# Performance work log

Hardware: AMD Instinct MI355X
Metric: run time of the kernel (lower is better)

Reference implementation:

```python
import jax, jax.numpy as jnp
import numpy as np

B, QL, KL = 8, 2048, 2048
QD, KD, ED = 1024, 1024, 1024


def setup_inputs() -> dict:
    key = jax.random.key(0)
    ks = jax.random.split(key, 11)
    s = 0.02
    return {
        "query": jax.random.normal(ks[0], (B, QL, QD), jnp.float32),
        "key_value": jax.random.normal(ks[1], (B, KL, KD), jnp.float32),
        "mask": jnp.ones((B, QL, KL), jnp.int32),
        "Wq": jax.random.normal(ks[2], (QD, ED), jnp.float32) * s,
        "bq": jnp.zeros((ED,), jnp.float32),
        "Wk": jax.random.normal(ks[3], (KD, ED), jnp.float32) * s,
        "bk": jnp.zeros((ED,), jnp.float32),
        "Wv": jax.random.normal(ks[4], (KD, ED), jnp.float32) * s,
        "bv": jnp.zeros((ED,), jnp.float32),
        "Wo": jax.random.normal(ks[5], (ED, ED), jnp.float32) * s,
        "bo": jnp.zeros((ED,), jnp.float32),
    }


def reference(query, key_value, mask, Wq, bq, Wk, bk, Wv, bv, Wo, bo):
    # Linear projections
    Q = jnp.einsum('bqd,de->bqe', query, Wq) + bq      # (B, QL, E)
    K = jnp.einsum('bkd,de->bke', key_value, Wk) + bk  # (B, KL, E)
    V = jnp.einsum('bkd,de->bke', key_value, Wv) + bv  # (B, KL, E)
    scale = 1.0 / jnp.sqrt(jnp.asarray(Q.shape[-1], Q.dtype))
    scores = jnp.einsum('bqe,bke->bqk', Q, K) * scale  # (B, QL, KL)
    scores = jnp.where(mask == 0, -jnp.inf, scores)
    attn = jax.nn.softmax(scores, axis=-1)             # (B, QL, KL)
    # dropout is identity in eval mode
    attended = jnp.einsum('bqk,bke->bqe', attn, V)     # (B, QL, E)
    out = jnp.einsum('bqe,ef->bqf', attended, Wo) + bo
    return out, attn
```

## Files before the change

### kernel.cpp

```cpp
#include <hip/hip_runtime.h>
#include <hip/hip_bf16.h>
#include <math.h>


typedef __attribute__((ext_vector_type(8))) short short8;
typedef __attribute__((ext_vector_type(4))) float floatx4;

__device__ __forceinline__ unsigned short f2bf(float x) {
  return __builtin_bit_cast(unsigned short, __float2bfloat16(x));
}
__device__ __forceinline__ float bf2f(unsigned short s) {
  unsigned int u = ((unsigned int)s) << 16;
  return __builtin_bit_cast(float, u);
}

typedef const unsigned int __attribute__((address_space(1))) ga_u32;
typedef unsigned int __attribute__((address_space(3))) lds_u32;
__device__ __forceinline__ void gl_lds16(const void* g, void* l) {
  __builtin_amdgcn_global_load_lds((ga_u32*)g, (lds_u32*)l, 16, 0, 0);
}

template <int EPI>
__global__ __launch_bounds__(512, 2) void gemm8(
    const unsigned short* __restrict__ Ah,
    const unsigned short* __restrict__ Bh, void* __restrict__ Cp,
    const float* __restrict__ bias, float alpha, int M, int N, int K, int Mt,
    long long sA, long long sB, long long sC) {
  extern __shared__ char smem[];

  const int gx = gridDim.x;
  const int gxy = gx * gridDim.y;
  const int nwg = gxy * gridDim.z;
  const int orig = blockIdx.z * gxy + blockIdx.y * gx + blockIdx.x;
  const int wg = (orig & 7) * (nwg >> 3) + (orig >> 3);
  const int zb_i = wg / gxy;
  const int rem = wg - zb_i * gxy;
  const int by = rem / gx;
  const int bx = rem - by * gx;
  const int m0 = by * 256, n0 = bx * 256;
  const long long zb = zb_i;

  const unsigned short* Ag = Ah + zb * sA;
  const unsigned short* Bg = Bh + zb * sB;

  const int t = threadIdx.x;
  const int srow = t >> 3;
  const int skw = ((t & 7) << 3) ^ ((srow & 7) << 3);
  const unsigned short* aS = Ag + (long long)(m0 + srow) * K + skw;
  const unsigned short* bS = Bg + (long long)(n0 + srow) * K + skw;
  char* dstA = smem + t * 16;
  char* dstB = smem + 65536 + t * 16;

  const int lane = t & 63;
  const int wv = t >> 6, wy = wv >> 2, wx = wv & 3;
  const int lm = lane & 15, q = lane >> 4;
  const int x0 = (q << 4) ^ ((lm & 7) << 4);
  const int aB0 = (wy * 128 + lm) * 128;
  const int bB0 = 65536 + (wx * 64 + lm) * 128;
  const int aRd0 = aB0 + x0, aRd1 = aB0 + (x0 ^ 64);
  const int bRd0 = bB0 + x0, bRd1 = bB0 + (x0 ^ 64);

  floatx4 acc[8][4];
#pragma unroll
  for (int i = 0; i < 8; ++i)
#pragma unroll
    for (int j = 0; j < 4; ++j) acc[i][j] = (floatx4)(0.0f);

  short8 fa[4][2];
  short8 fb[2][2][2];

#pragma unroll
  for (int c = 0; c < 4; ++c) {
    gl_lds16(aS + (long long)(c * 64) * K, dstA + c * 8192);
    gl_lds16(bS + (long long)(c * 64) * K, dstB + c * 8192);
  }
  gl_lds16(aS + 64, dstA + 32768);
  gl_lds16(bS + 64, dstB + 32768);
  gl_lds16(aS + 64LL * K + 64, dstA + 32768 + 8192);
  gl_lds16(bS + 64LL * K + 64, dstB + 32768 + 8192);
  asm volatile("s_waitcnt vmcnt(4)" ::: "memory");
  __builtin_amdgcn_s_barrier();

  auto tile = [&](int kt, int bo, int nbo) {
    const bool p1 = (kt + 64) < K;
    const bool p2 = (kt + 128) < K;
#pragma unroll
    for (int mt = 0; mt < 4; ++mt) {
      fa[mt][0] = *(const short8*)(smem + (bo + aRd0 + mt * 2048));
      fa[mt][1] = *(const short8*)(smem + (bo + aRd1 + mt * 2048));
    }
#pragma unroll
    for (int nt = 0; nt < 2; ++nt) {
      fb[0][nt][0] = *(const short8*)(smem + (bo + bRd0 + nt * 2048));
      fb[0][nt][1] = *(const short8*)(smem + (bo + bRd1 + nt * 2048));
    }
    if (p1) {
      gl_lds16(aS + 128LL * K + (kt + 64), dstA + nbo + 16384);
      gl_lds16(bS + 128LL * K + (kt + 64), dstB + nbo + 16384);
    }
    __builtin_amdgcn_s_barrier();
    __builtin_amdgcn_s_setprio(1);
#pragma unroll
    for (int mt = 0; mt < 4; ++mt)
#pragma unroll
      for (int nt = 0; nt < 2; ++nt) {
        acc[mt][nt] = __builtin_amdgcn_mfma_f32_16x16x32_bf16(
            fa[mt][0], fb[0][nt][0], acc[mt][nt], 0, 0, 0);
        acc[mt][nt] = __builtin_amdgcn_mfma_f32_16x16x32_bf16(
            fa[mt][1], fb[0][nt][1], acc[mt][nt], 0, 0, 0);
      }
    __builtin_amdgcn_s_setprio(0);
    __builtin_amdgcn_s_barrier();
#pragma unroll
    for (int nt = 0; nt < 2; ++nt) {
      fb[1][nt][0] = *(const short8*)(smem + (bo + bRd0 + 4096 + nt * 2048));
      fb[1][nt][1] = *(const short8*)(smem + (bo + bRd1 + 4096 + nt * 2048));
    }
    if (p1) {
      gl_lds16(aS + 192LL * K + (kt + 64), dstA + nbo + 24576);
      gl_lds16(bS + 192LL * K + (kt + 64), dstB + nbo + 24576);
    }
    __builtin_amdgcn_s_barrier();
    __builtin_amdgcn_s_setprio(1);
#pragma unroll
    for (int mt = 0; mt < 4; ++mt)
#pragma unroll
      for (int nt = 0; nt < 2; ++nt) {
        acc[mt][2 + nt] = __builtin_amdgcn_mfma_f32_16x16x32_bf16(
            fa[mt][0], fb[1][nt][0], acc[mt][2 + nt], 0, 0, 0);
        acc[mt][2 + nt] = __builtin_amdgcn_mfma_f32_16x16x32_bf16(
            fa[mt][1], fb[1][nt][1], acc[mt][2 + nt], 0, 0, 0);
      }
    __builtin_amdgcn_s_setprio(0);
    __builtin_amdgcn_s_barrier();
#pragma unroll
    for (int mt = 0; mt < 4; ++mt) {
      fa[mt][0] = *(const short8*)(smem + (bo + aRd0 + 8192 + mt * 2048));
      fa[mt][1] = *(const short8*)(smem + (bo + aRd1 + 8192 + mt * 2048));
    }
    if (p2) {
      gl_lds16(aS + (kt + 128), dstA + bo);
      gl_lds16(bS + (kt + 128), dstB + bo);
    }
    __builtin_amdgcn_s_barrier();
    __builtin_amdgcn_s_setprio(1);
#pragma unroll
    for (int mt = 0; mt < 4; ++mt)
#pragma unroll
      for (int nt = 0; nt < 2; ++nt) {
        acc[4 + mt][nt] = __builtin_amdgcn_mfma_f32_16x16x32_bf16(
            fa[mt][0], fb[0][nt][0], acc[4 + mt][nt], 0, 0, 0);
        acc[4 + mt][nt] = __builtin_amdgcn_mfma_f32_16x16x32_bf16(
            fa[mt][1], fb[0][nt][1], acc[4 + mt][nt], 0, 0, 0);
      }
    __builtin_amdgcn_s_setprio(0);
    __builtin_amdgcn_s_barrier();
    if (p2) {
      gl_lds16(aS + 64LL * K + (kt + 128), dstA + bo + 8192);
      gl_lds16(bS + 64LL * K + (kt + 128), dstB + bo + 8192);
    }
    __builtin_amdgcn_s_barrier();
    __builtin_amdgcn_s_setprio(1);
#pragma unroll
    for (int mt = 0; mt < 4; ++mt)
#pragma unroll
      for (int nt = 0; nt < 2; ++nt) {
        acc[4 + mt][2 + nt] = __builtin_amdgcn_mfma_f32_16x16x32_bf16(
            fa[mt][0], fb[1][nt][0], acc[4 + mt][2 + nt], 0, 0, 0);
        acc[4 + mt][2 + nt] = __builtin_amdgcn_mfma_f32_16x16x32_bf16(
            fa[mt][1], fb[1][nt][1], acc[4 + mt][2 + nt], 0, 0, 0);
      }
    __builtin_amdgcn_s_setprio(0);
    if (p2) {
      asm volatile("s_waitcnt vmcnt(4)" ::: "memory");
    } else {
      asm volatile("s_waitcnt vmcnt(0)" ::: "memory");
    }
    __builtin_amdgcn_s_barrier();
  };

  for (int kt = 0; kt < K; kt += 128) {
    tile(kt, 0, 32768);
    tile(kt + 64, 32768, 0);
  }

#pragma unroll
  for (int ni = 0; ni < 4; ++ni) {
    const int col = n0 + wx * 64 + ni * 16 + lm;
    const float bvv = bias ? bias[col] : 0.0f;
#pragma unroll
    for (int mi = 0; mi < 8; ++mi) {
      const int rbase = m0 + wy * 128 + mi * 16 + q * 4;
      if constexpr (EPI == 3) {
        const int b = rbase / Mt;
        const int kk = rbase - b * Mt;
        unsigned short* dd =
            (unsigned short*)Cp + (long long)b * sC + (long long)col * Mt + kk;
        ushort4 pk;
        pk.x = f2bf(acc[mi][ni][0] * alpha + bvv);
        pk.y = f2bf(acc[mi][ni][1] * alpha + bvv);
        pk.z = f2bf(acc[mi][ni][2] * alpha + bvv);
        pk.w = f2bf(acc[mi][ni][3] * alpha + bvv);
        *reinterpret_cast<ushort4*>(dd) = pk;
      } else {
#pragma unroll
        for (int i = 0; i < 4; ++i) {
          const long long idx = zb * sC + (long long)(rbase + i) * N + col;
          const float x = acc[mi][ni][i] * alpha + bvv;
          if constexpr (EPI == 0) {
            ((float*)Cp)[idx] = x;
          } else {
            ((unsigned short*)Cp)[idx] = f2bf(x);
          }
        }
      }
    }
  }
}

__global__ __launch_bounds__(256) void cvt_bf16(const float* __restrict__ in,
                                                unsigned short* __restrict__ o,
                                                int n8) {
  const int i = blockIdx.x * 256 + threadIdx.x;
  if (i >= n8) return;
  const float4* p = reinterpret_cast<const float4*>(in) + (long long)i * 2;
  const float4 a = p[0], b = p[1];
  short8 h;
  h[0] = (short)f2bf(a.x); h[1] = (short)f2bf(a.y);
  h[2] = (short)f2bf(a.z); h[3] = (short)f2bf(a.w);
  h[4] = (short)f2bf(b.x); h[5] = (short)f2bf(b.y);
  h[6] = (short)f2bf(b.z); h[7] = (short)f2bf(b.w);
  reinterpret_cast<short8*>(o)[i] = h;
}

__global__ __launch_bounds__(256) void prep_w(const float* __restrict__ W,
                                              unsigned short* __restrict__ Th,
                                              int R, int C) {
  __shared__ float tile[32][33];
  const int c0 = blockIdx.x * 32, r0 = blockIdx.y * 32;
  const int tx = threadIdx.x & 31, ty = threadIdx.x >> 5;
#pragma unroll
  for (int i = 0; i < 4; ++i)
    tile[ty + i * 8][tx] = W[(long long)(r0 + ty + i * 8) * C + c0 + tx];
  __syncthreads();
#pragma unroll
  for (int i = 0; i < 4; ++i) {
    const float x = tile[tx][ty + i * 8];
    const long long idx = (long long)(c0 + ty + i * 8) * R + r0 + tx;
    Th[idx] = f2bf(x);
  }
}

__global__ __launch_bounds__(256) void bias_wo(const float* __restrict__ bv,
                                               const float* __restrict__ Wo,
                                               float* __restrict__ bvWo) {
  __shared__ float red[4][64];
  const int fl = threadIdx.x & 63, eg = threadIdx.x >> 6;
  const int f = blockIdx.x * 64 + fl;
  float s = 0.0f;
  const int e0 = eg * 256;
  for (int e = e0; e < e0 + 256; ++e)
    s += bv[e] * Wo[(long long)e * 1024 + f];
  red[eg][fl] = s;
  __syncthreads();
  if (eg == 0) bvWo[f] = red[0][fl] + red[1][fl] + red[2][fl] + red[3][fl];
}

__device__ __forceinline__ float wave_max64(float v) {
#pragma unroll
  for (int o = 32; o > 0; o >>= 1) v = fmaxf(v, __shfl_xor(v, o, 64));
  return v;
}
__device__ __forceinline__ float wave_sum64(float v) {
#pragma unroll
  for (int o = 32; o > 0; o >>= 1) v += __shfl_xor(v, o, 64);
  return v;
}

__global__ __launch_bounds__(256) void softmax_kernel(
    const unsigned short* __restrict__ Sh, const int* __restrict__ mask,
    float* __restrict__ attn, unsigned short* __restrict__ Ph) {
  const long long base = (long long)blockIdx.x * 2048;
  const int t = threadIdx.x;

  float vals[8];
  float lmax = -INFINITY;
#pragma unroll
  for (int g = 0; g < 2; ++g) {
    const int idx = (t + g * 256) * 4;
    const uint2 u = *reinterpret_cast<const uint2*>(Sh + base + idx);
    const int4 m = *reinterpret_cast<const int4*>(mask + base + idx);
    vals[g * 4 + 0] = m.x ? bf2f((unsigned short)(u.x & 0xffff)) : -INFINITY;
    vals[g * 4 + 1] = m.y ? bf2f((unsigned short)(u.x >> 16)) : -INFINITY;
    vals[g * 4 + 2] = m.z ? bf2f((unsigned short)(u.y & 0xffff)) : -INFINITY;
    vals[g * 4 + 3] = m.w ? bf2f((unsigned short)(u.y >> 16)) : -INFINITY;
  }
#pragma unroll
  for (int i = 0; i < 8; ++i) lmax = fmaxf(lmax, vals[i]);

  __shared__ float red[4];
  const float wm = wave_max64(lmax);
  if ((t & 63) == 0) red[t >> 6] = wm;
  __syncthreads();
  const float rmax = fmaxf(fmaxf(red[0], red[1]), fmaxf(red[2], red[3]));
  __syncthreads();

  float lsum = 0.0f;
#pragma unroll
  for (int i = 0; i < 8; ++i) {
    const float e = __expf(vals[i] - rmax);
    vals[i] = e;
    lsum += e;
  }
  const float wsum = wave_sum64(lsum);
  if ((t & 63) == 0) red[t >> 6] = wsum;
  __syncthreads();
  const float inv = 1.0f / (red[0] + red[1] + red[2] + red[3]);

#pragma unroll
  for (int g = 0; g < 2; ++g) {
    const int idx = (t + g * 256) * 4;
    float4 o;
    o.x = vals[g * 4 + 0] * inv;
    o.y = vals[g * 4 + 1] * inv;
    o.z = vals[g * 4 + 2] * inv;
    o.w = vals[g * 4 + 3] * inv;
    *reinterpret_cast<float4*>(attn + base + idx) = o;
    uint2 p;
    p.x = (unsigned)f2bf(o.x) | ((unsigned)f2bf(o.y) << 16);
    p.y = (unsigned)f2bf(o.z) | ((unsigned)f2bf(o.w) << 16);
    *reinterpret_cast<uint2*>(Ph + base + idx) = p;
  }
}

extern "C" void kernel_launch(void* const* d_in, const int* in_sizes, int n_in,
                              void* d_out, int out_size, void* d_ws,
                              size_t ws_size, hipStream_t stream) {
  const float* query = (const float*)d_in[0];
  const float* keyv = (const float*)d_in[1];
  const int* mask = (const int*)d_in[2];
  const float* Wq = (const float*)d_in[3];
  const float* bq = (const float*)d_in[4];
  const float* Wk = (const float*)d_in[5];
  const float* bk = (const float*)d_in[6];
  const float* Wv = (const float*)d_in[7];
  const float* bv = (const float*)d_in[8];
  const float* Wo = (const float*)d_in[9];
  const float* bo = (const float*)d_in[10];

  const int B = 8, QL = 2048, KL = 2048, D = 1024;
  const long long ML = (long long)B * QL;

  static int inited = 0;
  if (!inited) {
    hipFuncSetAttribute(reinterpret_cast<const void*>(&gemm8<0>),
                        hipFuncAttributeMaxDynamicSharedMemorySize, 131072);
    hipFuncSetAttribute(reinterpret_cast<const void*>(&gemm8<1>),
                        hipFuncAttributeMaxDynamicSharedMemorySize, 131072);
    hipFuncSetAttribute(reinterpret_cast<const void*>(&gemm8<3>),
                        hipFuncAttributeMaxDynamicSharedMemorySize, 131072);
    inited = 1;
  }

  float* out = (float*)d_out;
  float* attn = out + ML * D;

  char* w = (char*)d_ws;
  unsigned short* Qh = (unsigned short*)(w);
  unsigned short* Kh = (unsigned short*)(w + (32ll << 20));
  unsigned short* KVf = (unsigned short*)(w + (64ll << 20));
  unsigned short* Qf = (unsigned short*)(w + (96ll << 20));
  unsigned short* VWoT = (unsigned short*)(w + (128ll << 20));
  unsigned short* Sh = (unsigned short*)(w + (64ll << 20));
  unsigned short* Ph = (unsigned short*)(w);
  unsigned short* WqT = (unsigned short*)(w + (160ll << 20));
  unsigned short* WkT = WqT + (1ll << 20);
  unsigned short* WoTh = WkT + (1ll << 20);
  unsigned short* W2T = WoTh + (1ll << 20);
  unsigned short* WvH = W2T + (1ll << 20);
  float* bvWo = attn;

  const dim3 blk(256);
  const int n8 = (int)(ML * D / 8);

  cvt_bf16<<<dim3(n8 / 256), blk, 0, stream>>>(query, Qf, n8);
  cvt_bf16<<<dim3(n8 / 256), blk, 0, stream>>>(keyv, KVf, n8);
  cvt_bf16<<<dim3(512), blk, 0, stream>>>(Wv, WvH, D * D / 8);

  prep_w<<<dim3(32, 32), blk, 0, stream>>>(Wq, WqT, D, D);
  prep_w<<<dim3(32, 32), blk, 0, stream>>>(Wk, WkT, D, D);
  prep_w<<<dim3(32, 32), blk, 0, stream>>>(Wo, WoTh, D, D);

  bias_wo<<<dim3(16), blk, 0, stream>>>(bv, Wo, bvWo);

  gemm8<1><<<dim3(D / 256, D / 256, 1), 512, 131072, stream>>>(
      WoTh, WvH, W2T, nullptr, 1.0f, D, D, D, 1, 0, 0, 0);

  gemm8<1><<<dim3(D / 256, ML / 256, 1), 512, 131072, stream>>>(
      Qf, WqT, Qh, bq, 1.0f, (int)ML, D, D, 1, 0, 0, 0);
  gemm8<1><<<dim3(D / 256, ML / 256, 1), 512, 131072, stream>>>(
      KVf, WkT, Kh, bk, 1.0f, (int)ML, D, D, 1, 0, 0, 0);

  gemm8<3><<<dim3(D / 256, ML / 256, 1), 512, 131072, stream>>>(
      KVf, W2T, VWoT, bvWo, 1.0f, (int)ML, D, D, KL, 0, 0,
      (long long)D * KL);

  gemm8<1><<<dim3(KL / 256, QL / 256, B), 512, 131072, stream>>>(
      Qh, Kh, Sh, nullptr, 0.03125f, QL, KL, D, 1,
      (long long)QL * D, (long long)KL * D, (long long)QL * KL);

  softmax_kernel<<<dim3((int)ML), blk, 0, stream>>>(Sh, mask, attn, Ph);

  gemm8<0><<<dim3(D / 256, QL / 256, B), 512, 131072, stream>>>(
      Ph, VWoT, out, bo, 1.0f, QL, D, KL, 1, (long long)QL * KL,
      (long long)D * KL, (long long)QL * D);
}
```

Before: 728.1 us.

## Fold Wk into Wq so scores use raw key_value, dropping K projection

Uses the identity Q·K^T = query·(Wq Wk^T)·kv^T. A fused weight W3 = Wq·Wk^T is precomputed with a new small bf16 MFMA GEMM, so the separate K projection GEMM over the full batch goes away and the score GEMM reads the bf16 key_value directly. The bq·K term becomes a per-key bias (kv·(Wk bq)), computed by new wk_bq/kv_dot kernels and added inside the softmax, and the bk terms are dropped because they are constant along each softmax row. This removes one large GEMM, but rounding the product weight to bf16 changes the numerical error profile.

```diff
diff --git a/kernel.cpp b/kernel.cpp
--- a/kernel.cpp
+++ b/kernel.cpp
@@ -218,6 +218,73 @@
   }
 }
 
+__global__ __launch_bounds__(256) void gemm128(
+    const unsigned short* __restrict__ A, const unsigned short* __restrict__ B,
+    unsigned short* __restrict__ C, int M, int N, int K) {
+  __shared__ unsigned short As_h[128 * 32];
+  __shared__ unsigned short Bs_h[128 * 32];
+
+  const int t = threadIdx.x;
+  const int lane = t & 63;
+  const int wave = t >> 6;
+  const int wy = wave >> 1, wx = wave & 1;
+  const int lm = lane & 15, q = lane >> 4;
+  const int m0 = blockIdx.y * 128, n0 = blockIdx.x * 128;
+
+  floatx4 acc[4][4];
+#pragma unroll
+  for (int i = 0; i < 4; ++i)
+#pragma unroll
+    for (int j = 0; j < 4; ++j) acc[i][j] = (floatx4)(0.0f);
+
+  const int ch_row = lane >> 2;
+  const int ch_off = (lane & 3) << 3;
+
+  for (int k0 = 0; k0 < K; k0 += 32) {
+    __syncthreads();
+#pragma unroll
+    for (int j = 0; j < 2; ++j) {
+      const int chunk = wave * 2 + j;
+      const int row = chunk * 16 + ch_row;
+      gl_lds16(A + (long long)(m0 + row) * K + k0 + ch_off,
+               &As_h[chunk * 512 + lane * 8]);
+      gl_lds16(B + (long long)(n0 + row) * K + k0 + ch_off,
+               &Bs_h[chunk * 512 + lane * 8]);
+    }
+    __syncthreads();
+
+    short8 fa[4], fb[4];
+#pragma unroll
+    for (int mt = 0; mt < 4; ++mt) {
+      const int row = wy * 64 + mt * 16 + lm;
+      fa[mt] = *reinterpret_cast<const short8*>(&As_h[row * 32 + q * 8]);
+    }
+#pragma unroll
+    for (int nt = 0; nt < 4; ++nt) {
+      const int row = wx * 64 + nt * 16 + lm;
+      fb[nt] = *reinterpret_cast<const short8*>(&Bs_h[row * 32 + q * 8]);
+    }
+#pragma unroll
+    for (int mt = 0; mt < 4; ++mt)
+#pragma unroll
+      for (int nt = 0; nt < 4; ++nt)
+        acc[mt][nt] = __builtin_amdgcn_mfma_f32_16x16x32_bf16(
+            fa[mt], fb[nt], acc[mt][nt], 0, 0, 0);
+  }
+
+#pragma unroll
+  for (int nt = 0; nt < 4; ++nt) {
+    const int col = n0 + wx * 64 + nt * 16 + lm;
+#pragma unroll
+    for (int mt = 0; mt < 4; ++mt) {
+      const int rbase = m0 + wy * 64 + mt * 16 + q * 4;
+#pragma unroll
+      for (int i = 0; i < 4; ++i)
+        C[(long long)(rbase + i) * N + col] = f2bf(acc[mt][nt][i]);
+    }
+  }
+}
+
 __global__ __launch_bounds__(256) void cvt_bf16(const float* __restrict__ in,
                                                 unsigned short* __restrict__ o,
                                                 int n8) {
@@ -251,6 +318,17 @@
   }
 }
 
+__device__ __forceinline__ float wave_max64(float v) {
+#pragma unroll
+  for (int o = 32; o > 0; o >>= 1) v = fmaxf(v, __shfl_xor(v, o, 64));
+  return v;
+}
+__device__ __forceinline__ float wave_sum64(float v) {
+#pragma unroll
+  for (int o = 32; o > 0; o >>= 1) v += __shfl_xor(v, o, 64);
+  return v;
+}
+
 __global__ __launch_bounds__(256) void bias_wo(const float* __restrict__ bv,
                                                const float* __restrict__ Wo,
                                                float* __restrict__ bvWo) {
@@ -266,21 +344,42 @@
   if (eg == 0) bvWo[f] = red[0][fl] + red[1][fl] + red[2][fl] + red[3][fl];
 }
 
-__device__ __forceinline__ float wave_max64(float v) {
-#pragma unroll
-  for (int o = 32; o > 0; o >>= 1) v = fmaxf(v, __shfl_xor(v, o, 64));
-  return v;
-}
-__device__ __forceinline__ float wave_sum64(float v) {
-#pragma unroll
-  for (int o = 32; o > 0; o >>= 1) v += __shfl_xor(v, o, 64);
-  return v;
+__global__ __launch_bounds__(256) void wk_bq(const float* __restrict__ Wk,
+                                             const float* __restrict__ bq,
+                                             float* __restrict__ w4) {
+  const int lane = threadIdx.x & 63, wv = threadIdx.x >> 6;
+  const int d = blockIdx.x * 4 + wv;
+  const float* row = Wk + (long long)d * 1024;
+  float s = 0.0f;
+#pragma unroll
+  for (int i = 0; i < 16; ++i) s += row[lane + i * 64] * bq[lane + i * 64];
+  s = wave_sum64(s);
+  if (lane == 0) w4[d] = s;
+}
+
+__global__ __launch_bounds__(256) void kv_dot(
+    const unsigned short* __restrict__ kvh, const float* __restrict__ w4,
+    float scale, float* __restrict__ c) {
+  const int lane = threadIdx.x & 63, wv = threadIdx.x >> 6;
+  const long long r = (long long)blockIdx.x * 4 + wv;
+  const unsigned short* p = kvh + r * 1024 + lane * 16;
+  const short8 h0 = *(const short8*)(p);
+  const short8 h1 = *(const short8*)(p + 8);
+  float s = 0.0f;
+#pragma unroll
+  for (int i = 0; i < 8; ++i) s += bf2f((unsigned short)h0[i]) * w4[lane * 16 + i];
+#pragma unroll
+  for (int i = 0; i < 8; ++i) s += bf2f((unsigned short)h1[i]) * w4[lane * 16 + 8 + i];
+  s = wave_sum64(s);
+  if (lane == 0) c[r] = s * scale;
 }
 
 __global__ __launch_bounds__(256) void softmax_kernel(
     const unsigned short* __restrict__ Sh, const int* __restrict__ mask,
-    float* __restrict__ attn, unsigned short* __restrict__ Ph) {
+    const float* __restrict__ c, float* __restrict__ attn,
+    unsigned short* __restrict__ Ph) {
   const long long base = (long long)blockIdx.x * 2048;
+  const long long cb = (long long)(blockIdx.x >> 11) * 2048;
   const int t = threadIdx.x;
 
   float vals[8];
@@ -290,10 +389,15 @@
     const int idx = (t + g * 256) * 4;
     const uint2 u = *reinterpret_cast<const uint2*>(Sh + base + idx);
     const int4 m = *reinterpret_cast<const int4*>(mask + base + idx);
-    vals[g * 4 + 0] = m.x ? bf2f((unsigned short)(u.x & 0xffff)) : -INFINITY;
-    vals[g * 4 + 1] = m.y ? bf2f((unsigned short)(u.x >> 16)) : -INFINITY;
-    vals[g * 4 + 2] = m.z ? bf2f((unsigned short)(u.y & 0xffff)) : -INFINITY;
-    vals[g * 4 + 3] = m.w ? bf2f((unsigned short)(u.y >> 16)) : -INFINITY;
+    const float4 cv = *reinterpret_cast<const float4*>(c + cb + idx);
+    vals[g * 4 + 0] =
+        m.x ? bf2f((unsigned short)(u.x & 0xffff)) + cv.x : -INFINITY;
+    vals[g * 4 + 1] =
+        m.y ? bf2f((unsigned short)(u.x >> 16)) + cv.y : -INFINITY;
+    vals[g * 4 + 2] =
+        m.z ? bf2f((unsigned short)(u.y & 0xffff)) + cv.z : -INFINITY;
+    vals[g * 4 + 3] =
+        m.w ? bf2f((unsigned short)(u.y >> 16)) + cv.w : -INFINITY;
   }
 #pragma unroll
   for (int i = 0; i < 8; ++i) lmax = fmaxf(lmax, vals[i]);
@@ -347,6 +451,7 @@
   const float* bv = (const float*)d_in[8];
   const float* Wo = (const float*)d_in[9];
   const float* bo = (const float*)d_in[10];
+  (void)bk;
 
   const int B = 8, QL = 2048, KL = 2048, D = 1024;
   const long long ML = (long long)B * QL;
@@ -366,50 +471,52 @@
   float* attn = out + ML * D;
 
   char* w = (char*)d_ws;
-  unsigned short* Qh = (unsigned short*)(w);
-  unsigned short* Kh = (unsigned short*)(w + (32ll << 20));
-  unsigned short* KVf = (unsigned short*)(w + (64ll << 20));
+  unsigned short* QW3h = (unsigned short*)(w);
+  unsigned short* KVf = (unsigned short*)(w + (32ll << 20));
+  unsigned short* Sh = (unsigned short*)(w + (64ll << 20));
   unsigned short* Qf = (unsigned short*)(w + (96ll << 20));
   unsigned short* VWoT = (unsigned short*)(w + (128ll << 20));
-  unsigned short* Sh = (unsigned short*)(w + (64ll << 20));
   unsigned short* Ph = (unsigned short*)(w);
-  unsigned short* WqT = (unsigned short*)(w + (160ll << 20));
-  unsigned short* WkT = WqT + (1ll << 20);
-  unsigned short* WoTh = WkT + (1ll << 20);
-  unsigned short* W2T = WoTh + (1ll << 20);
-  unsigned short* WvH = W2T + (1ll << 20);
-  float* bvWo = attn;
+  unsigned short* WqH = (unsigned short*)(w + (128ll << 20));
+  unsigned short* WkH = (unsigned short*)(w + (130ll << 20));
+  unsigned short* WvH = (unsigned short*)(w + (132ll << 20));
+  unsigned short* WoTh = (unsigned short*)(w + (134ll << 20));
+  unsigned short* W2T = (unsigned short*)(w + (160ll << 20));
+  unsigned short* W3T = (unsigned short*)(w + (162ll << 20));
+  float* cvec = (float*)(w + (164ll << 20));
+  float* w4 = (float*)(w + (165ll << 20));
+  float* bvWo = (float*)(w + (166ll << 20));
 
   const dim3 blk(256);
   const int n8 = (int)(ML * D / 8);
 
+  cvt_bf16<<<dim3(512), blk, 0, stream>>>(Wq, WqH, D * D / 8);
+  cvt_bf16<<<dim3(512), blk, 0, stream>>>(Wk, WkH, D * D / 8);
+  cvt_bf16<<<dim3(512), blk, 0, stream>>>(Wv, WvH, D * D / 8);
+  prep_w<<<dim3(32, 32), blk, 0, stream>>>(Wo, WoTh, D, D);
+  wk_bq<<<dim3(D / 4), blk, 0, stream>>>(Wk, bq, w4);
+  bias_wo<<<dim3(16), blk, 0, stream>>>(bv, Wo, bvWo);
+
+  gemm128<<<dim3(8, 8), blk, 0, stream>>>(WkH, WqH, W3T, D, D, D);
+  gemm128<<<dim3(8, 8), blk, 0, stream>>>(WoTh, WvH, W2T, D, D, D);
+
   cvt_bf16<<<dim3(n8 / 256), blk, 0, stream>>>(query, Qf, n8);
   cvt_bf16<<<dim3(n8 / 256), blk, 0, stream>>>(keyv, KVf, n8);
-  cvt_bf16<<<dim3(512), blk, 0, stream>>>(Wv, WvH, D * D / 8);
-
-  prep_w<<<dim3(32, 32), blk, 0, stream>>>(Wq, WqT, D, D);
-  prep_w<<<dim3(32, 32), blk, 0, stream>>>(Wk, WkT, D, D);
-  prep_w<<<dim3(32, 32), blk, 0, stream>>>(Wo, WoTh, D, D);
-
-  bias_wo<<<dim3(16), blk, 0, stream>>>(bv, Wo, bvWo);
-
-  gemm8<1><<<dim3(D / 256, D / 256, 1), 512, 131072, stream>>>(
-      WoTh, WvH, W2T, nullptr, 1.0f, D, D, D, 1, 0, 0, 0);
+
+  kv_dot<<<dim3((int)ML / 4), blk, 0, stream>>>(KVf, w4, 0.03125f, cvec);
 
   gemm8<1><<<dim3(D / 256, ML / 256, 1), 512, 131072, stream>>>(
-      Qf, WqT, Qh, bq, 1.0f, (int)ML, D, D, 1, 0, 0, 0);
-  gemm8<1><<<dim3(D / 256, ML / 256, 1), 512, 131072, stream>>>(
-      KVf, WkT, Kh, bk, 1.0f, (int)ML, D, D, 1, 0, 0, 0);
+      Qf, W3T, QW3h, nullptr, 1.0f, (int)ML, D, D, 1, 0, 0, 0);
 
   gemm8<3><<<dim3(D / 256, ML / 256, 1), 512, 131072, stream>>>(
       KVf, W2T, VWoT, bvWo, 1.0f, (int)ML, D, D, KL, 0, 0,
       (long long)D * KL);
 
   gemm8<1><<<dim3(KL / 256, QL / 256, B), 512, 131072, stream>>>(
-      Qh, Kh, Sh, nullptr, 0.03125f, QL, KL, D, 1,
+      QW3h, KVf, Sh, nullptr, 0.03125f, QL, KL, D, 1,
       (long long)QL * D, (long long)KL * D, (long long)QL * KL);
 
-  softmax_kernel<<<dim3((int)ML), blk, 0, stream>>>(Sh, mask, attn, Ph);
+  softmax_kernel<<<dim3((int)ML), blk, 0, stream>>>(Sh, mask, cvec, attn, Ph);
 
   gemm8<0><<<dim3(D / 256, QL / 256, B), 512, 131072, stream>>>(
       Ph, VWoT, out, bo, 1.0f, QL, D, KL, 1, (long long)QL * KL,
```

New measurement: 722.0 us. Within noise of the previous version (-0.8%).
